# Kernel tuning notes

Measured on AMD Instinct MI355X. Metric: run time of the kernel, lower is better.

The kernel has to match this reference:

```python
import jax, jax.numpy as jnp
import numpy as np

N_EMBD = 2048
HEAD_SIZE = 128

def setup_inputs() -> dict:
    key = jax.random.key(0)
    kx, kk, kq, kv = jax.random.split(key, 4)
    bound = 1.0 / np.sqrt(N_EMBD)  # torch Linear default init range
    x = jax.random.normal(kx, (4, 4096, N_EMBD), dtype=jnp.float32)
    Wk = jax.random.uniform(kk, (N_EMBD, HEAD_SIZE), jnp.float32, -bound, bound)
    Wq = jax.random.uniform(kq, (N_EMBD, HEAD_SIZE), jnp.float32, -bound, bound)
    Wv = jax.random.uniform(kv, (N_EMBD, HEAD_SIZE), jnp.float32, -bound, bound)
    return {"x": x, "Wk": Wk, "Wq": Wq, "Wv": Wv}

def reference(x, Wk, Wq, Wv):
    B, T, C = x.shape
    k = jnp.einsum('btc,ch->bth', x, Wk)
    q = jnp.einsum('btc,ch->bth', x, Wq)
    v = jnp.einsum('btc,ch->bth', x, Wv)
    # NOTE: original scales by C**-0.5 where C = n_embd (input dim), not head_size
    scores = jnp.einsum('bth,bsh->bts', q, k) * (C ** -0.5)
    causal = jnp.tril(jnp.ones((T, T), dtype=bool))  # [T,T]
    scores = jnp.where(causal, scores, -jnp.inf)
    probs = jax.nn.softmax(scores, axis=-1)
    # dropout_probability = 0.0 -> identity
    return jnp.einsum('bts,bsh->bth', probs, v)
```

## Files before the change

kernel.cpp:

```cpp
#include <hip/hip_runtime.h>
#include <hip/hip_bf16.h>

#define T_SEQ 4096
#define NB 4
#define CEMB 2048
#define HS 128

typedef __attribute__((ext_vector_type(8))) short bf16x8;
typedef __attribute__((ext_vector_type(4))) float f32x4;
typedef __attribute__((ext_vector_type(16))) float f32x16;

__device__ inline short f2bf(float f) {
    union { float f; unsigned u; } v; v.f = f;
    unsigned r = v.u + 0x7FFFu + ((v.u >> 16) & 1u);
    return (short)(r >> 16);
}

__device__ inline unsigned pk2(float lo, float hi) {
    return ((unsigned)(unsigned short)f2bf(lo)) | (((unsigned)(unsigned short)f2bf(hi)) << 16);
}

__device__ inline void gld16(const void* gsrc, void* lds) {
    __builtin_amdgcn_global_load_lds(
        (const __attribute__((address_space(1))) unsigned*)gsrc,
        (__attribute__((address_space(3))) unsigned*)lds, 16, 0, 0);
}

__global__ __launch_bounds__(256) void wt_kernel(
    const float* __restrict__ Wq, const float* __restrict__ Wk,
    const float* __restrict__ Wv, short* __restrict__ Wt) {
    int d = blockIdx.x * 256 + threadIdx.x;
    int mat = d >> 18;
    int rm  = d & 262143;
    int s   = rm >> 13;
    int e   = rm & 8191;
    int p   = e * 2;
    int n   = p >> 7;
    int lin = p ^ ((n & 7) << 4);
    int kk  = (lin & 127) >> 1;
    int k   = s * 64 + kk;
    const float* W = (mat == 0) ? Wq : (mat == 1) ? Wk : Wv;
    Wt[d] = f2bf(W[k * HS + n]);
}

__global__ __launch_bounds__(256, 3) void proj_kernel(
    const float* __restrict__ x, const short* __restrict__ Wt,
    short* __restrict__ qg, short* __restrict__ kg, short* __restrict__ vtg) {
    __shared__ short Wlds[3][8192];

    const int tid = threadIdx.x;
    const int w   = tid >> 6;
    const int l   = tid & 63;
    const int lg  = l >> 4;
    const int lr  = l & 15;

    const int bid = blockIdx.x;
    const int wk  = (bid & 7) * 96 + (bid >> 3);
    const int mat = wk % 3;
    const int m0  = (wk / 3) * 64;

    const short* Wp = Wt + (long)mat * 262144;

    f32x4 acc[8];
    #pragma unroll
    for (int b = 0; b < 8; b++) acc[b] = (f32x4){0.f, 0.f, 0.f, 0.f};

    const float* xrow = x + (long)(m0 + w * 16 + lr) * CEMB;
    const int sw = (lr & 7) << 4;

    float4 xs[3][4];

#define STAGE(S, B) do {                                                   \
        const short* gp_ = Wp + (long)(S) * 8192 + (long)(w * 4) * 512 + l * 8; \
        gld16(gp_,        &Wlds[B][(w * 4 + 0) * 512]);                    \
        gld16(gp_ + 512,  &Wlds[B][(w * 4 + 1) * 512]);                    \
        gld16(gp_ + 1024, &Wlds[B][(w * 4 + 2) * 512]);                    \
        gld16(gp_ + 1536, &Wlds[B][(w * 4 + 3) * 512]);                    \
    } while (0)

#define LOADX(S, B) do {                                                   \
        const float* xn_ = xrow + (S) * 64;                                \
        xs[B][0] = *reinterpret_cast<const float4*>(xn_ + lg * 8);         \
        xs[B][1] = *reinterpret_cast<const float4*>(xn_ + lg * 8 + 4);     \
        xs[B][2] = *reinterpret_cast<const float4*>(xn_ + 32 + lg * 8);    \
        xs[B][3] = *reinterpret_cast<const float4*>(xn_ + 32 + lg * 8 + 4);\
    } while (0)

    STAGE(0, 0);
    LOADX(0, 0);
    STAGE(1, 1);
    LOADX(1, 1);

#define STEP(S, B0, B2) do {                                               \
        asm volatile("s_waitcnt vmcnt(8) lgkmcnt(0)\n\ts_barrier" ::: "memory"); \
        if ((S) + 2 < 32) { STAGE((S) + 2, B2); LOADX((S) + 2, B2); }      \
        bf16x8 a0, a1;                                                     \
        a0[0] = f2bf(xs[B0][0].x); a0[1] = f2bf(xs[B0][0].y);              \
        a0[2] = f2bf(xs[B0][0].z); a0[3] = f2bf(xs[B0][0].w);              \
        a0[4] = f2bf(xs[B0][1].x); a0[5] = f2bf(xs[B0][1].y);              \
        a0[6] = f2bf(xs[B0][1].z); a0[7] = f2bf(xs[B0][1].w);              \
        a1[0] = f2bf(xs[B0][2].x); a1[1] = f2bf(xs[B0][2].y);              \
        a1[2] = f2bf(xs[B0][2].z); a1[3] = f2bf(xs[B0][2].w);              \
        a1[4] = f2bf(xs[B0][3].x); a1[5] = f2bf(xs[B0][3].y);              \
        a1[6] = f2bf(xs[B0][3].z); a1[7] = f2bf(xs[B0][3].w);              \
        const char* lbase_ = (const char*)&Wlds[B0][0];                    \
        _Pragma("unroll")                                                  \
        for (int nt = 0; nt < 8; nt++) {                                   \
            int off_ = (((nt * 16 + lr) * 128 + lg * 16)) ^ sw;            \
            bf16x8 bfr_ = *reinterpret_cast<const bf16x8*>(lbase_ + off_); \
            acc[nt] = __builtin_amdgcn_mfma_f32_16x16x32_bf16(             \
                a0, bfr_, acc[nt], 0, 0, 0);                               \
        }                                                                  \
        _Pragma("unroll")                                                  \
        for (int nt = 0; nt < 8; nt++) {                                   \
            int off_ = (((nt * 16 + lr) * 128 + lg * 16 + 64)) ^ sw;       \
            bf16x8 bfr_ = *reinterpret_cast<const bf16x8*>(lbase_ + off_); \
            acc[nt] = __builtin_amdgcn_mfma_f32_16x16x32_bf16(             \
                a1, bfr_, acc[nt], 0, 0, 0);                               \
        }                                                                  \
    } while (0)

    for (int s = 0; s < 30; s += 3) {
        STEP(s, 0, 2);
        STEP(s + 1, 1, 0);
        STEP(s + 2, 2, 1);
    }
    STEP(30, 0, 2);
    STEP(31, 1, 0);

#undef STEP
#undef LOADX
#undef STAGE

    if (mat == 0) {
        const float scale = 0.0318793851f;
        #pragma unroll
        for (int nt = 0; nt < 8; nt++)
            #pragma unroll
            for (int r = 0; r < 4; r++) {
                int row = m0 + w * 16 + lg * 4 + r;
                qg[(long)row * HS + nt * 16 + lr] = f2bf(acc[nt][r] * scale);
            }
    } else if (mat == 1) {
        #pragma unroll
        for (int nt = 0; nt < 8; nt++)
            #pragma unroll
            for (int r = 0; r < 4; r++) {
                int row = m0 + w * 16 + lg * 4 + r;
                kg[(long)row * HS + nt * 16 + lr] = f2bf(acc[nt][r]);
            }
    } else {
        #pragma unroll
        for (int nt = 0; nt < 8; nt++)
            #pragma unroll
            for (int r = 0; r < 4; r++) {
                int row = m0 + w * 16 + lg * 4 + r;
                int b   = row >> 12;
                int tl  = row & 4095;
                vtg[(long)b * (HS * T_SEQ) + (long)(nt * 16 + lr) * T_SEQ + tl]
                    = f2bf(acc[nt][r]);
            }
    }
}

__global__ __launch_bounds__(256, 2) void attn_kernel(
    const short* __restrict__ qg, const short* __restrict__ kg,
    const short* __restrict__ vtg, float* __restrict__ out) {
    __shared__ float Lacc[4][32][128];
    __shared__ float Lm[4][32];
    __shared__ float Ll[4][32];

    const int tid = threadIdx.x;
    const int w   = tid >> 6;
    const int l   = tid & 63;
    const int c31 = l & 31;
    const int hi  = l >> 5;
    const int hi4 = hi << 2;
    const int hi8 = hi << 3;

    const int bid = blockIdx.x;
    const int xcd = bid & 7;
    const int idx = bid >> 3;
    const int b   = xcd >> 1;
    const int qt  = 127 - ((idx << 1) | (xcd & 1));
    const int q0  = qt * 32;
    const int qrow = q0 + c31;

    const short* kb = kg  + (long)b * T_SEQ * HS;
    const short* vb = vtg + (long)b * HS * T_SEQ;

    bf16x8 qf[8];
    #pragma unroll
    for (int kc = 0; kc < 8; kc++)
        qf[kc] = *reinterpret_cast<const bf16x8*>(
            &qg[(long)(b * T_SEQ + qrow) * HS + kc * 16 + hi8]);

    f32x16 accO[4];
    #pragma unroll
    for (int nb = 0; nb < 4; nb++)
        #pragma unroll
        for (int i = 0; i < 16; i++) accO[nb][i] = 0.f;
    float mrow = -__builtin_inff();
    float lsum = 0.f;

    const int ntk = (qt >> 1) + 1;

    #pragma unroll 1
    for (int t = w; t < ntk; t += 4) {
        const int kv0 = t * 64;

        f32x16 SA, SB;
        #pragma unroll
        for (int i = 0; i < 16; i++) { SA[i] = 0.f; SB[i] = 0.f; }
        #pragma unroll
        for (int kc = 0; kc < 8; kc++) {
            bf16x8 ka = *reinterpret_cast<const bf16x8*>(
                &kb[(long)(kv0 + c31) * HS + kc * 16 + hi8]);
            bf16x8 kbf = *reinterpret_cast<const bf16x8*>(
                &kb[(long)(kv0 + 32 + c31) * HS + kc * 16 + hi8]);
            SA = __builtin_amdgcn_mfma_f32_32x32x16_bf16(ka,  qf[kc], SA, 0, 0, 0);
            SB = __builtin_amdgcn_mfma_f32_32x32x16_bf16(kbf, qf[kc], SB, 0, 0, 0);
        }

        float pA[16], pB[16];
        #pragma unroll
        for (int r = 0; r < 16; r++) { pA[r] = SA[r]; pB[r] = SB[r]; }

        if (kv0 + 63 > q0) {
            #pragma unroll
            for (int r = 0; r < 16; r++) {
                int kr = kv0 + (r & 3) + 8 * (r >> 2) + hi4;
                pA[r] = (kr > qrow)      ? -__builtin_inff() : pA[r];
                pB[r] = (kr + 32 > qrow) ? -__builtin_inff() : pB[r];
            }
        }

        float t16[16];
        #pragma unroll
        for (int r = 0; r < 16; r++) t16[r] = fmaxf(pA[r], pB[r]);
        #pragma unroll
        for (int s2 = 8; s2 >= 1; s2 >>= 1)
            #pragma unroll
            for (int r = 0; r < 8; r++)
                if (r < s2) t16[r] = fmaxf(t16[r], t16[r + s2]);
        float mt   = fmaxf(t16[0], __shfl_xor(t16[0], 32));
        float mnew = fmaxf(mrow, mt);
        float fac  = exp2f(mrow - mnew);

        #pragma unroll
        for (int r = 0; r < 16; r++) {
            pA[r] = exp2f(pA[r] - mnew);
            pB[r] = exp2f(pB[r] - mnew);
        }
        float s16[16];
        #pragma unroll
        for (int r = 0; r < 16; r++) s16[r] = pA[r] + pB[r];
        #pragma unroll
        for (int s2 = 8; s2 >= 1; s2 >>= 1)
            #pragma unroll
            for (int r = 0; r < 8; r++)
                if (r < s2) s16[r] += s16[r + s2];
        float ts = s16[0] + __shfl_xor(s16[0], 32);
        lsum = lsum * fac + ts;
        mrow = mnew;

        #pragma unroll
        for (int nb = 0; nb < 4; nb++)
            #pragma unroll
            for (int i = 0; i < 16; i++) accO[nb][i] *= fac;

        bf16x8 pf[4];
        #pragma unroll
        for (int kc = 0; kc < 4; kc++) {
            const int V0 = 2 * kc, V1 = 2 * kc + 1;
            const int r0 = ((V0 >> 2) << 4) | ((V0 & 3) << 2);
            const int r1 = ((V1 >> 2) << 4) | ((V1 & 3) << 2);
#define PSEL(i) ((i) < 16 ? pA[(i) & 15] : pB[(i) & 15])
            unsigned a0 = pk2(PSEL(r0 + 0), PSEL(r0 + 1));
            unsigned a1 = pk2(PSEL(r0 + 2), PSEL(r0 + 3));
            unsigned b0 = pk2(PSEL(r1 + 0), PSEL(r1 + 1));
            unsigned b1 = pk2(PSEL(r1 + 2), PSEL(r1 + 3));
#undef PSEL
            unsigned k0 = hi ? b0 : a0, k1 = hi ? b1 : a1;
            unsigned s0 = hi ? a0 : b0, s1 = hi ? a1 : b1;
            unsigned g0 = (unsigned)__shfl_xor((int)s0, 32);
            unsigned g1 = (unsigned)__shfl_xor((int)s1, 32);
            union { unsigned u[4]; bf16x8 v; } U;
            U.u[0] = hi ? g0 : k0;
            U.u[1] = hi ? g1 : k1;
            U.u[2] = hi ? k0 : g0;
            U.u[3] = hi ? k1 : g1;
            pf[kc] = U.v;
        }

        #pragma unroll
        for (int kc = 0; kc < 4; kc++) {
            #pragma unroll
            for (int nb = 0; nb < 4; nb++) {
                bf16x8 vf = *reinterpret_cast<const bf16x8*>(
                    &vb[(long)(nb * 32 + c31) * T_SEQ + kv0 + kc * 16 + hi8]);
                accO[nb] = __builtin_amdgcn_mfma_f32_32x32x16_bf16(
                    pf[kc], vf, accO[nb], 0, 0, 0);
            }
        }
    }

    #pragma unroll
    for (int nb = 0; nb < 4; nb++)
        #pragma unroll
        for (int r = 0; r < 16; r++)
            Lacc[w][(r & 3) + 8 * (r >> 2) + hi4][nb * 32 + c31] = accO[nb][r];
    if (l < 32) { Lm[w][c31] = mrow; Ll[w][c31] = lsum; }
    __syncthreads();

    {
        const int row = tid >> 3;
        const int c0  = (tid & 7) * 16;
        float m0 = Lm[0][row], m1 = Lm[1][row], m2 = Lm[2][row], m3 = Lm[3][row];
        float ms = fmaxf(fmaxf(m0, m1), fmaxf(m2, m3));
        float f0 = exp2f(m0 - ms), f1 = exp2f(m1 - ms);
        float f2 = exp2f(m2 - ms), f3 = exp2f(m3 - ms);
        float L = Ll[0][row] * f0 + Ll[1][row] * f1 + Ll[2][row] * f2 + Ll[3][row] * f3;
        float inv = 1.0f / L;
        float* op = &out[((long)b * T_SEQ + q0 + row) * HS + c0];
        #pragma unroll
        for (int j = 0; j < 16; j++) {
            float o = Lacc[0][row][c0 + j] * f0 + Lacc[1][row][c0 + j] * f1
                    + Lacc[2][row][c0 + j] * f2 + Lacc[3][row][c0 + j] * f3;
            op[j] = o * inv;
        }
    }
}

extern "C" void kernel_launch(void* const* d_in, const int* in_sizes, int n_in,
                              void* d_out, int out_size, void* d_ws, size_t ws_size,
                              hipStream_t stream) {
    const float* x  = (const float*)d_in[0];
    const float* Wk = (const float*)d_in[1];
    const float* Wq = (const float*)d_in[2];
    const float* Wv = (const float*)d_in[3];
    float* out = (float*)d_out;

    char* ws = (char*)d_ws;
    short* Wt  = (short*)ws;
    short* qg  = (short*)(ws + 1572864);
    short* kg  = (short*)(ws + 1572864 + 4194304);
    short* vtg = (short*)(ws + 1572864 + 8388608);

    wt_kernel  <<<3072, 256, 0, stream>>>(Wq, Wk, Wv, Wt);
    proj_kernel<<<768,  256, 0, stream>>>(x, Wt, qg, kg, vtg);
    attn_kernel<<<512,  256, 0, stream>>>(qg, kg, vtg, out);
}
```

Measured before the change: 163.5 us.

## Prefetch K/V fragments ahead of MFMAs, skip redundant rescale, use hardware bf16 pack

Batch-loads all K fragments and half of the V fragments before the QK^T MFMA chain, and issues the remaining V loads during the softmax, so global-load latency overlaps compute instead of stalling each MFMA. The online-softmax rescale of the output accumulator is skipped when no row max increases. The manual bf16 rounding is replaced with the v_cvt_pk_bf16_f32 instruction, and s_setprio is raised around the MFMA blocks. Holding more live fragments raises VGPR pressure, which could lower occupancy, and Q is now reloaded on every iteration.

Result: no change. 162.1 us (-0.9%).

```diff
diff --git a/kernel.cpp b/kernel.cpp
--- a/kernel.cpp
+++ b/kernel.cpp
@@ -17,7 +17,9 @@
 }
 
 __device__ inline unsigned pk2(float lo, float hi) {
-    return ((unsigned)(unsigned short)f2bf(lo)) | (((unsigned)(unsigned short)f2bf(hi)) << 16);
+    unsigned r;
+    asm("v_cvt_pk_bf16_f32 %0, %1, %2" : "=v"(r) : "v"(lo), "v"(hi));
+    return r;
 }
 
 __device__ inline void gld16(const void* gsrc, void* lds) {
@@ -188,12 +190,7 @@
 
     const short* kb = kg  + (long)b * T_SEQ * HS;
     const short* vb = vtg + (long)b * HS * T_SEQ;
-
-    bf16x8 qf[8];
-    #pragma unroll
-    for (int kc = 0; kc < 8; kc++)
-        qf[kc] = *reinterpret_cast<const bf16x8*>(
-            &qg[(long)(b * T_SEQ + qrow) * HS + kc * 16 + hi8]);
+    const short* qb = qg  + (long)(b * T_SEQ + qrow) * HS;
 
     f32x16 accO[4];
     #pragma unroll
@@ -209,18 +206,39 @@
     for (int t = w; t < ntk; t += 4) {
         const int kv0 = t * 64;
 
+        bf16x8 ka[8], kb2[8];
+        #pragma unroll
+        for (int kc = 0; kc < 8; kc++)
+            ka[kc] = *reinterpret_cast<const bf16x8*>(
+                &kb[(long)(kv0 + c31) * HS + kc * 16 + hi8]);
+        #pragma unroll
+        for (int kc = 0; kc < 8; kc++)
+            kb2[kc] = *reinterpret_cast<const bf16x8*>(
+                &kb[(long)(kv0 + 32 + c31) * HS + kc * 16 + hi8]);
+
+        bf16x8 qf[8];
+        #pragma unroll
+        for (int kc = 0; kc < 8; kc++)
+            qf[kc] = *reinterpret_cast<const bf16x8*>(&qb[kc * 16 + hi8]);
+
+        bf16x8 vfA[2][4];
+        #pragma unroll
+        for (int kc = 0; kc < 2; kc++)
+            #pragma unroll
+            for (int nb = 0; nb < 4; nb++)
+                vfA[kc][nb] = *reinterpret_cast<const bf16x8*>(
+                    &vb[(long)(nb * 32 + c31) * T_SEQ + kv0 + kc * 16 + hi8]);
+
         f32x16 SA, SB;
         #pragma unroll
         for (int i = 0; i < 16; i++) { SA[i] = 0.f; SB[i] = 0.f; }
+        __builtin_amdgcn_s_setprio(1);
         #pragma unroll
         for (int kc = 0; kc < 8; kc++) {
-            bf16x8 ka = *reinterpret_cast<const bf16x8*>(
-                &kb[(long)(kv0 + c31) * HS + kc * 16 + hi8]);
-            bf16x8 kbf = *reinterpret_cast<const bf16x8*>(
-                &kb[(long)(kv0 + 32 + c31) * HS + kc * 16 + hi8]);
-            SA = __builtin_amdgcn_mfma_f32_32x32x16_bf16(ka,  qf[kc], SA, 0, 0, 0);
-            SB = __builtin_amdgcn_mfma_f32_32x32x16_bf16(kbf, qf[kc], SB, 0, 0, 0);
-        }
+            SA = __builtin_amdgcn_mfma_f32_32x32x16_bf16(ka[kc],  qf[kc], SA, 0, 0, 0);
+            SB = __builtin_amdgcn_mfma_f32_32x32x16_bf16(kb2[kc], qf[kc], SB, 0, 0, 0);
+        }
+        __builtin_amdgcn_s_setprio(0);
 
         float pA[16], pB[16];
         #pragma unroll
@@ -243,14 +261,31 @@
             #pragma unroll
             for (int r = 0; r < 8; r++)
                 if (r < s2) t16[r] = fmaxf(t16[r], t16[r + s2]);
-        float mt   = fmaxf(t16[0], __shfl_xor(t16[0], 32));
-        float mnew = fmaxf(mrow, mt);
-        float fac  = exp2f(mrow - mnew);
+        float mt = fmaxf(t16[0], __shfl_xor(t16[0], 32));
+
+        if (__any(mt > mrow)) {
+            float mnew = fmaxf(mrow, mt);
+            float fac  = exp2f(mrow - mnew);
+            lsum *= fac;
+            #pragma unroll
+            for (int nb = 0; nb < 4; nb++)
+                #pragma unroll
+                for (int i = 0; i < 16; i++) accO[nb][i] *= fac;
+            mrow = mnew;
+        }
+
+        bf16x8 vfB[2][4];
+        #pragma unroll
+        for (int kc = 0; kc < 2; kc++)
+            #pragma unroll
+            for (int nb = 0; nb < 4; nb++)
+                vfB[kc][nb] = *reinterpret_cast<const bf16x8*>(
+                    &vb[(long)(nb * 32 + c31) * T_SEQ + kv0 + (kc + 2) * 16 + hi8]);
 
         #pragma unroll
         for (int r = 0; r < 16; r++) {
-            pA[r] = exp2f(pA[r] - mnew);
-            pB[r] = exp2f(pB[r] - mnew);
+            pA[r] = exp2f(pA[r] - mrow);
+            pB[r] = exp2f(pB[r] - mrow);
         }
         float s16[16];
         #pragma unroll
@@ -260,14 +295,7 @@
             #pragma unroll
             for (int r = 0; r < 8; r++)
                 if (r < s2) s16[r] += s16[r + s2];
-        float ts = s16[0] + __shfl_xor(s16[0], 32);
-        lsum = lsum * fac + ts;
-        mrow = mnew;
-
-        #pragma unroll
-        for (int nb = 0; nb < 4; nb++)
-            #pragma unroll
-            for (int i = 0; i < 16; i++) accO[nb][i] *= fac;
+        lsum += s16[0] + __shfl_xor(s16[0], 32);
 
         bf16x8 pf[4];
         #pragma unroll
@@ -293,16 +321,20 @@
             pf[kc] = U.v;
         }
 
-        #pragma unroll
-        for (int kc = 0; kc < 4; kc++) {
-            #pragma unroll
-            for (int nb = 0; nb < 4; nb++) {
-                bf16x8 vf = *reinterpret_cast<const bf16x8*>(
-                    &vb[(long)(nb * 32 + c31) * T_SEQ + kv0 + kc * 16 + hi8]);
-                accO[nb] = __builtin_amdgcn_mfma_f32_32x32x16_bf16(
-                    pf[kc], vf, accO[nb], 0, 0, 0);
-            }
-        }
+        __builtin_amdgcn_s_setprio(1);
+        #pragma unroll
+        for (int nb = 0; nb < 4; nb++)
+            accO[nb] = __builtin_amdgcn_mfma_f32_32x32x16_bf16(pf[0], vfA[0][nb], accO[nb], 0, 0, 0);
+        #pragma unroll
+        for (int nb = 0; nb < 4; nb++)
+            accO[nb] = __builtin_amdgcn_mfma_f32_32x32x16_bf16(pf[1], vfA[1][nb], accO[nb], 0, 0, 0);
+        #pragma unroll
+        for (int nb = 0; nb < 4; nb++)
+            accO[nb] = __builtin_amdgcn_mfma_f32_32x32x16_bf16(pf[2], vfB[0][nb], accO[nb], 0, 0, 0);
+        #pragma unroll
+        for (int nb = 0; nb < 4; nb++)
+            accO[nb] = __builtin_amdgcn_mfma_f32_32x32x16_bf16(pf[3], vfB[1][nb], accO[nb], 0, 0, 0);
+        __builtin_amdgcn_s_setprio(0);
     }
 
     #pragma unroll
```
